# Performance work log

Measured on AMD Instinct MI355X. Metric: run time of the kernel, lower is better.

Reference implementation:

```python
import jax, jax.numpy as jnp
import numpy as np

DIM = 1024
RANK = 16


def setup_inputs() -> dict:
    key = jax.random.key(0)
    ks = jax.random.split(key, 9)
    s = 0.02
    return {
        "x": jax.random.normal(ks[0], (2, 4096, DIM), dtype=jnp.float32),
        "W_qkv": jax.random.normal(ks[1], (3 * DIM, DIM), dtype=jnp.float32) * s,
        "b_qkv": jax.random.normal(ks[2], (3 * DIM,), dtype=jnp.float32) * s,
        "A_q": jax.random.normal(ks[3], (RANK, DIM), dtype=jnp.float32) * s,
        "B_q": jax.random.normal(ks[4], (DIM, RANK), dtype=jnp.float32) * s,
        "A_k": jax.random.normal(ks[5], (RANK, DIM), dtype=jnp.float32) * s,
        "B_k": jax.random.normal(ks[6], (DIM, RANK), dtype=jnp.float32) * s,
        "A_v": jax.random.normal(ks[7], (RANK, DIM), dtype=jnp.float32) * s,
        "B_v": jax.random.normal(ks[8], (DIM, RANK), dtype=jnp.float32) * s,
        "alpha": jnp.float32(0.5),
    }


def reference(x, W_qkv, b_qkv, A_q, B_q, A_k, B_k, A_v, B_v, alpha):
    # base fused QKV projection: [B, S, 3*dim]
    qkv = jnp.einsum("bsd,od->bso", x, W_qkv) + b_qkv
    # low-rank adapters: x @ A.T @ B.T, rank=16
    lora_q = jnp.einsum("bsr,dr->bsd", jnp.einsum("bsd,rd->bsr", x, A_q), B_q)
    lora_k = jnp.einsum("bsr,dr->bsd", jnp.einsum("bsd,rd->bsr", x, A_k), B_k)
    lora_v = jnp.einsum("bsr,dr->bsd", jnp.einsum("bsd,rd->bsr", x, A_v), B_v)
    # scaled add into q/k/v slices (concat order matches torch slice layout)
    delta = jnp.concatenate([lora_q, lora_k, lora_v], axis=-1)
    return qkv + alpha * delta
```

## Files before the change

### kernel.cpp

```cpp
#include <hip/hip_runtime.h>
#include <stdint.h>

#define DIM    1024
#define RANK   16
#define M_TOT  8192
#define N_TOT  3072
#define K_TOT  1024

#define BM 256
#define BN 128
#define BK 64
#define NT (K_TOT / BK)

typedef __attribute__((ext_vector_type(8))) short  s8v;
typedef __attribute__((ext_vector_type(4))) float  f4v;

__device__ __forceinline__ unsigned short f2bf(float f) {
    union { float f; unsigned int u; } v; v.f = f;
    unsigned int u = v.u;
    u += 0x7FFFu + ((u >> 16) & 1u);
    return (unsigned short)(u >> 16);
}

__device__ __forceinline__ void gload_lds16(const unsigned short* g,
                                            unsigned short* l) {
    __builtin_amdgcn_global_load_lds(
        (const __attribute__((address_space(1))) void*)g,
        (__attribute__((address_space(3))) void*)l,
        16, 0, 0);
}

__global__ __launch_bounds__(256)
void prep(const float4* __restrict__ x, ushort4* __restrict__ xb,
          const float* __restrict__ W,
          const float* __restrict__ Aq, const float* __restrict__ Bq,
          const float* __restrict__ Ak, const float* __restrict__ Bk,
          const float* __restrict__ Av, const float* __restrict__ Bv,
          const float* __restrict__ alpha_p,
          unsigned short* __restrict__ Wb) {
    const int tid = threadIdx.x;
    if (blockIdx.x < 2048) {
        int i = blockIdx.x * 256 + tid;
        #pragma unroll
        for (int k = 0; k < 4; ++k) {
            float4 v = x[i];
            ushort4 o;
            o.x = f2bf(v.x); o.y = f2bf(v.y); o.z = f2bf(v.z); o.w = f2bf(v.w);
            xb[i] = o;
            i += 2048 * 256;
        }
    } else {
        const int bid2 = blockIdx.x - 2048;
        const int sel  = bid2 >> 6;
        const int rb   = bid2 & 63;
        const float* Am = (sel == 0) ? Aq : (sel == 1) ? Ak : Av;
        const float* Bm = (sel == 0) ? Bq : (sel == 1) ? Bk : Bv;

        __shared__ float sb[16][RANK];
        {
            const int row = rb * 16 + (tid >> 4);
            sb[tid >> 4][tid & 15] = alpha_p[0] * Bm[row * RANK + (tid & 15)];
        }
        __syncthreads();

        float4 a4[RANK];
        #pragma unroll
        for (int r = 0; r < RANK; ++r)
            a4[r] = ((const float4*)(Am + r * DIM))[tid];

        #pragma unroll
        for (int row = 0; row < 16; ++row) {
            const int o = sel * 1024 + rb * 16 + row;
            float4 w = ((const float4*)(W + (size_t)o * DIM))[tid];
            #pragma unroll
            for (int r = 0; r < RANK; ++r) {
                const float s = sb[row][r];
                w.x += s * a4[r].x; w.y += s * a4[r].y;
                w.z += s * a4[r].z; w.w += s * a4[r].w;
            }
            ushort4 ov;
            ov.x = f2bf(w.x); ov.y = f2bf(w.y); ov.z = f2bf(w.z); ov.w = f2bf(w.w);
            ((ushort4*)(Wb + (size_t)o * DIM))[tid] = ov;
        }
    }
}

__global__ __launch_bounds__(512, 2)
void gemm_bt(const unsigned short* __restrict__ Xb,
             const unsigned short* __restrict__ Wb,
             const float* __restrict__ bias,
             float* __restrict__ out) {
    __shared__ __align__(16) unsigned short As[2][BM * BK];
    __shared__ __align__(16) unsigned short Bs[2][BN * BK];

    const int tid  = threadIdx.x;
    const int wave = tid >> 6;
    const int lane = tid & 63;
    const int l15  = lane & 15;
    const int lq   = lane >> 4;
    const int wr   = wave >> 1;
    const int wc   = wave & 1;

    const int bid = blockIdx.x;
    const int xcd = bid & 7;
    const int s   = bid >> 3;
    const int bn  = s % 24;
    const int bm  = xcd * 4 + s / 24;

    const unsigned short* aptr[4];
    const unsigned short* bptr[2];
    int aoff[4], boff[2];
    #pragma unroll
    for (int u = 0; u < 4; ++u) {
        const int c   = wave * 4 + u;
        const int row = ((c >> 1) << 4) + l15;
        const int col = ((c & 1) << 5) + (lq << 3);
        aptr[u] = Xb + (size_t)(bm * BM + row) * K_TOT + col;
        aoff[u] = c * 512;
    }
    #pragma unroll
    for (int u = 0; u < 2; ++u) {
        const int c   = wave * 2 + u;
        const int row = ((c >> 1) << 4) + l15;
        const int col = ((c & 1) << 5) + (lq << 3);
        bptr[u] = Wb + (size_t)(bn * BN + row) * K_TOT + col;
        boff[u] = c * 512;
    }

    #pragma unroll
    for (int t = 0; t < 2; ++t) {
        #pragma unroll
        for (int u = 0; u < 4; ++u) gload_lds16(aptr[u] + t * BK, &As[t][aoff[u]]);
        #pragma unroll
        for (int u = 0; u < 2; ++u) gload_lds16(bptr[u] + t * BK, &Bs[t][boff[u]]);
    }

    f4v acc[4][4] = {};

    #define COMPUTE(curbuf)                                                      \
    {                                                                            \
        const s8v* Avp = (const s8v*)As[curbuf];                                 \
        const s8v* Bvp = (const s8v*)Bs[curbuf];                                 \
        _Pragma("unroll")                                                        \
        for (int t = 0; t < 2; ++t) {                                            \
            s8v af[4], bf[4];                                                    \
            _Pragma("unroll")                                                    \
            for (int i = 0; i < 4; ++i) {                                        \
                af[i] = Avp[((wr * 4 + i) * 2 + t) * 64 + lane];                 \
                bf[i] = Bvp[((wc * 4 + i) * 2 + t) * 64 + lane];                 \
            }                                                                    \
            _Pragma("unroll")                                                    \
            for (int i = 0; i < 4; ++i)                                          \
                _Pragma("unroll")                                                \
                for (int j = 0; j < 4; ++j)                                      \
                    acc[i][j] = __builtin_amdgcn_mfma_f32_16x16x32_bf16(         \
                        af[i], bf[j], acc[i][j], 0, 0, 0);                       \
        }                                                                        \
    }

    #pragma unroll 2
    for (int kt = 0; kt < NT - 2; ++kt) {
        const int cur = kt & 1;
        asm volatile("s_waitcnt vmcnt(6)" ::: "memory");
        __builtin_amdgcn_sched_barrier(0);
        __builtin_amdgcn_s_barrier();
        __builtin_amdgcn_sched_barrier(0);

        COMPUTE(cur);

        __builtin_amdgcn_sched_barrier(0);
        __builtin_amdgcn_s_barrier();
        __builtin_amdgcn_sched_barrier(0);

        #pragma unroll
        for (int u = 0; u < 4; ++u)
            gload_lds16(aptr[u] + (kt + 2) * BK, &As[cur][aoff[u]]);
        #pragma unroll
        for (int u = 0; u < 2; ++u)
            gload_lds16(bptr[u] + (kt + 2) * BK, &Bs[cur][boff[u]]);
    }

    asm volatile("s_waitcnt vmcnt(6)" ::: "memory");
    __builtin_amdgcn_sched_barrier(0);
    __builtin_amdgcn_s_barrier();
    __builtin_amdgcn_sched_barrier(0);
    COMPUTE(0);

    asm volatile("s_waitcnt vmcnt(0)" ::: "memory");
    __builtin_amdgcn_sched_barrier(0);
    __builtin_amdgcn_s_barrier();
    __builtin_amdgcn_sched_barrier(0);
    COMPUTE(1);
    #undef COMPUTE

    const int col_base = bn * BN + wc * 64;
    const int row_base = bm * BM + wr * 64 + lq * 4;
    #pragma unroll
    for (int j = 0; j < 4; ++j) {
        const int col = col_base + j * 16 + l15;
        const float bv = bias[col];
        #pragma unroll
        for (int i = 0; i < 4; ++i) {
            const int row = row_base + i * 16;
            #pragma unroll
            for (int r = 0; r < 4; ++r)
                out[(size_t)(row + r) * N_TOT + col] = acc[i][j][r] + bv;
        }
    }
}

extern "C" void kernel_launch(void* const* d_in, const int* in_sizes, int n_in,
                              void* d_out, int out_size, void* d_ws, size_t ws_size,
                              hipStream_t stream) {
    const float* x     = (const float*)d_in[0];
    const float* W     = (const float*)d_in[1];
    const float* b     = (const float*)d_in[2];
    const float* Aq    = (const float*)d_in[3];
    const float* Bq    = (const float*)d_in[4];
    const float* Ak    = (const float*)d_in[5];
    const float* Bk    = (const float*)d_in[6];
    const float* Av    = (const float*)d_in[7];
    const float* Bv    = (const float*)d_in[8];
    const float* alpha = (const float*)d_in[9];
    float* out = (float*)d_out;

    unsigned short* xb = (unsigned short*)d_ws;
    unsigned short* Wb = (unsigned short*)((char*)d_ws + (size_t)M_TOT * K_TOT * 2);

    prep<<<2048 + 192, 256, 0, stream>>>((const float4*)x, (ushort4*)xb,
                                         W, Aq, Bq, Ak, Bk, Av, Bv, alpha, Wb);

    gemm_bt<<<(M_TOT / BM) * (N_TOT / BN), 512, 0, stream>>>(xb, Wb, b, out);
}
```

Baseline: 254.0 us.

## Triple-buffer LDS and interleave async loads with MFMA sub-steps in GEMM

Switches the GEMM main loop from a double-buffered LDS ring to a three-stage ring, so the prefetch for tile q+2 can be issued while tile q is being consumed, with no barrier needed before overwriting. The global-to-LDS loads are split across the two K sub-steps and interleaved with the LDS fragment reads, and MFMA sections are wrapped in s_setprio for higher wave priority. This aims to hide memory latency and reduce barrier stalls. In exchange it raises LDS use to 144KB per block, which may limit occupancy to one block per CU, and the loop is no longer unrolled.

```diff
diff --git a/kernel.cpp b/kernel.cpp
--- a/kernel.cpp
+++ b/kernel.cpp
@@ -90,8 +90,8 @@
              const unsigned short* __restrict__ Wb,
              const float* __restrict__ bias,
              float* __restrict__ out) {
-    __shared__ __align__(16) unsigned short As[2][BM * BK];
-    __shared__ __align__(16) unsigned short Bs[2][BN * BK];
+    __shared__ __align__(16) unsigned short As[3][BM * BK];
+    __shared__ __align__(16) unsigned short Bs[3][BN * BK];
 
     const int tid  = threadIdx.x;
     const int wave = tid >> 6;
@@ -134,64 +134,86 @@
         #pragma unroll
         for (int u = 0; u < 2; ++u) gload_lds16(bptr[u] + t * BK, &Bs[t][boff[u]]);
     }
-
-    f4v acc[4][4] = {};
-
-    #define COMPUTE(curbuf)                                                      \
-    {                                                                            \
-        const s8v* Avp = (const s8v*)As[curbuf];                                 \
-        const s8v* Bvp = (const s8v*)Bs[curbuf];                                 \
-        _Pragma("unroll")                                                        \
-        for (int t = 0; t < 2; ++t) {                                            \
-            s8v af[4], bf[4];                                                    \
-            _Pragma("unroll")                                                    \
-            for (int i = 0; i < 4; ++i) {                                        \
-                af[i] = Avp[((wr * 4 + i) * 2 + t) * 64 + lane];                 \
-                bf[i] = Bvp[((wc * 4 + i) * 2 + t) * 64 + lane];                 \
-            }                                                                    \
-            _Pragma("unroll")                                                    \
-            for (int i = 0; i < 4; ++i)                                          \
-                _Pragma("unroll")                                                \
-                for (int j = 0; j < 4; ++j)                                      \
-                    acc[i][j] = __builtin_amdgcn_mfma_f32_16x16x32_bf16(         \
-                        af[i], bf[j], acc[i][j], 0, 0, 0);                       \
-        }                                                                        \
-    }
-
-    #pragma unroll 2
-    for (int kt = 0; kt < NT - 2; ++kt) {
-        const int cur = kt & 1;
-        asm volatile("s_waitcnt vmcnt(6)" ::: "memory");
-        __builtin_amdgcn_sched_barrier(0);
-        __builtin_amdgcn_s_barrier();
-        __builtin_amdgcn_sched_barrier(0);
-
-        COMPUTE(cur);
-
-        __builtin_amdgcn_sched_barrier(0);
-        __builtin_amdgcn_s_barrier();
-        __builtin_amdgcn_sched_barrier(0);
-
-        #pragma unroll
-        for (int u = 0; u < 4; ++u)
-            gload_lds16(aptr[u] + (kt + 2) * BK, &As[cur][aoff[u]]);
-        #pragma unroll
-        for (int u = 0; u < 2; ++u)
-            gload_lds16(bptr[u] + (kt + 2) * BK, &Bs[cur][boff[u]]);
-    }
-
     asm volatile("s_waitcnt vmcnt(6)" ::: "memory");
     __builtin_amdgcn_sched_barrier(0);
     __builtin_amdgcn_s_barrier();
     __builtin_amdgcn_sched_barrier(0);
-    COMPUTE(0);
-
-    asm volatile("s_waitcnt vmcnt(0)" ::: "memory");
-    __builtin_amdgcn_sched_barrier(0);
-    __builtin_amdgcn_s_barrier();
-    __builtin_amdgcn_sched_barrier(0);
-    COMPUTE(1);
-    #undef COMPUTE
+
+    f4v acc[4][4] = {};
+
+    #pragma unroll 1
+    for (int q = 0; q < NT; ++q) {
+        const int r    = q % 3;
+        const int r2   = (q + 2) % 3;
+        const int kg   = (q + 2) * BK;
+        const bool iss = (q + 2) < NT;
+        const s8v* Avp = (const s8v*)As[r];
+        const s8v* Bvp = (const s8v*)Bs[r];
+
+        {
+            s8v af[4], bf[4];
+            #pragma unroll
+            for (int i = 0; i < 4; ++i) {
+                af[i] = Avp[((wr * 4 + i) * 2 + 0) * 64 + lane];
+                bf[i] = Bvp[((wc * 4 + i) * 2 + 0) * 64 + lane];
+            }
+            if (iss) {
+                gload_lds16(aptr[0] + kg, &As[r2][aoff[0]]);
+                gload_lds16(aptr[1] + kg, &As[r2][aoff[1]]);
+                gload_lds16(bptr[0] + kg, &Bs[r2][boff[0]]);
+            }
+            __builtin_amdgcn_sched_barrier(0);
+            __builtin_amdgcn_s_barrier();
+            asm volatile("s_waitcnt lgkmcnt(0)" ::: "memory");
+            __builtin_amdgcn_sched_barrier(0);
+            __builtin_amdgcn_s_setprio(1);
+            #pragma unroll
+            for (int i = 0; i < 4; ++i)
+                #pragma unroll
+                for (int j = 0; j < 4; ++j)
+                    acc[i][j] = __builtin_amdgcn_mfma_f32_16x16x32_bf16(
+                        af[i], bf[j], acc[i][j], 0, 0, 0);
+            __builtin_amdgcn_s_setprio(0);
+            __builtin_amdgcn_sched_barrier(0);
+            __builtin_amdgcn_s_barrier();
+            __builtin_amdgcn_sched_barrier(0);
+        }
+
+        {
+            s8v af[4], bf[4];
+            #pragma unroll
+            for (int i = 0; i < 4; ++i) {
+                af[i] = Avp[((wr * 4 + i) * 2 + 1) * 64 + lane];
+                bf[i] = Bvp[((wc * 4 + i) * 2 + 1) * 64 + lane];
+            }
+            if (iss) {
+                gload_lds16(aptr[2] + kg, &As[r2][aoff[2]]);
+                gload_lds16(aptr[3] + kg, &As[r2][aoff[3]]);
+                gload_lds16(bptr[1] + kg, &Bs[r2][boff[1]]);
+            }
+            __builtin_amdgcn_sched_barrier(0);
+            __builtin_amdgcn_s_barrier();
+            asm volatile("s_waitcnt lgkmcnt(0)" ::: "memory");
+            __builtin_amdgcn_sched_barrier(0);
+            __builtin_amdgcn_s_setprio(1);
+            #pragma unroll
+            for (int i = 0; i < 4; ++i)
+                #pragma unroll
+                for (int j = 0; j < 4; ++j)
+                    acc[i][j] = __builtin_amdgcn_mfma_f32_16x16x32_bf16(
+                        af[i], bf[j], acc[i][j], 0, 0, 0);
+            __builtin_amdgcn_s_setprio(0);
+            __builtin_amdgcn_sched_barrier(0);
+            if (q < NT - 2) {
+                asm volatile("s_waitcnt vmcnt(6)" ::: "memory");
+            } else if (q == NT - 2) {
+                asm volatile("s_waitcnt vmcnt(0)" ::: "memory");
+            }
+            __builtin_amdgcn_sched_barrier(0);
+            __builtin_amdgcn_s_barrier();
+            __builtin_amdgcn_sched_barrier(0);
+        }
+    }
 
     const int col_base = bn * BN + wc * 64;
     const int row_base = bm * BM + wr * 64 + lq * 4;
```

New measurement: 233.4 us. 8.1% less time.

## Use 256x256 tiles with a 4-slot LDS ring and one barrier per step

Applied to the files above, without the earlier changes.

The GEMM tile grows from 256x128 to 256x256 and BK drops to 32. The two double buffers become one 4-slot LDS ring that keeps three stages of global-to-LDS loads in flight, with a single barrier per k-step. Waves are arranged 2x4, each computing a 128x64 sub-tile, and the MFMA bursts are raised with s_setprio. The aim is more reuse per LDS byte, fewer barriers and deeper latency hiding. The cost is 128KB of LDS, which allows only one block per CU, more accumulator registers per wave, and half as many blocks, which may hurt load balance across CUs.

```diff
diff --git a/kernel.cpp b/kernel.cpp
--- a/kernel.cpp
+++ b/kernel.cpp
@@ -8,9 +8,13 @@
 #define K_TOT  1024
 
 #define BM 256
-#define BN 128
-#define BK 64
+#define BN 256
+#define BK 32
 #define NT (K_TOT / BK)
+#define SLOT_H   16384
+#define SLOT_V   2048
+#define B_OFF_H  8192
+#define B_OFF_V  1024
 
 typedef __attribute__((ext_vector_type(8))) short  s8v;
 typedef __attribute__((ext_vector_type(4))) float  f4v;
@@ -90,117 +94,105 @@
              const unsigned short* __restrict__ Wb,
              const float* __restrict__ bias,
              float* __restrict__ out) {
-    __shared__ __align__(16) unsigned short As[2][BM * BK];
-    __shared__ __align__(16) unsigned short Bs[2][BN * BK];
+    __shared__ __align__(16) unsigned short S[4 * SLOT_H];
 
     const int tid  = threadIdx.x;
     const int wave = tid >> 6;
     const int lane = tid & 63;
     const int l15  = lane & 15;
     const int lq   = lane >> 4;
-    const int wr   = wave >> 1;
-    const int wc   = wave & 1;
+    const int wr   = wave >> 2;
+    const int wc   = wave & 3;
 
     const int bid = blockIdx.x;
     const int xcd = bid & 7;
     const int s   = bid >> 3;
-    const int bn  = s % 24;
-    const int bm  = xcd * 4 + s / 24;
-
-    const unsigned short* aptr[4];
+    const int bm  = xcd * 4 + s / 12;
+    const int bn  = s % 12;
+
+    const unsigned short* aptr[2];
     const unsigned short* bptr[2];
-    int aoff[4], boff[2];
-    #pragma unroll
-    for (int u = 0; u < 4; ++u) {
-        const int c   = wave * 4 + u;
-        const int row = ((c >> 1) << 4) + l15;
-        const int col = ((c & 1) << 5) + (lq << 3);
-        aptr[u] = Xb + (size_t)(bm * BM + row) * K_TOT + col;
-        aoff[u] = c * 512;
-    }
+    int aoff[2], boff[2];
     #pragma unroll
     for (int u = 0; u < 2; ++u) {
         const int c   = wave * 2 + u;
-        const int row = ((c >> 1) << 4) + l15;
-        const int col = ((c & 1) << 5) + (lq << 3);
+        const int row = c * 16 + l15;
+        const int col = lq << 3;
+        aptr[u] = Xb + (size_t)(bm * BM + row) * K_TOT + col;
         bptr[u] = Wb + (size_t)(bn * BN + row) * K_TOT + col;
-        boff[u] = c * 512;
-    }
-
-    #pragma unroll
-    for (int t = 0; t < 2; ++t) {
-        #pragma unroll
-        for (int u = 0; u < 4; ++u) gload_lds16(aptr[u] + t * BK, &As[t][aoff[u]]);
-        #pragma unroll
-        for (int u = 0; u < 2; ++u) gload_lds16(bptr[u] + t * BK, &Bs[t][boff[u]]);
-    }
-
-    f4v acc[4][4] = {};
-
-    #define COMPUTE(curbuf)                                                      \
-    {                                                                            \
-        const s8v* Avp = (const s8v*)As[curbuf];                                 \
-        const s8v* Bvp = (const s8v*)Bs[curbuf];                                 \
-        _Pragma("unroll")                                                        \
-        for (int t = 0; t < 2; ++t) {                                            \
-            s8v af[4], bf[4];                                                    \
-            _Pragma("unroll")                                                    \
-            for (int i = 0; i < 4; ++i) {                                        \
-                af[i] = Avp[((wr * 4 + i) * 2 + t) * 64 + lane];                 \
-                bf[i] = Bvp[((wc * 4 + i) * 2 + t) * 64 + lane];                 \
-            }                                                                    \
-            _Pragma("unroll")                                                    \
-            for (int i = 0; i < 4; ++i)                                          \
-                _Pragma("unroll")                                                \
-                for (int j = 0; j < 4; ++j)                                      \
-                    acc[i][j] = __builtin_amdgcn_mfma_f32_16x16x32_bf16(         \
-                        af[i], bf[j], acc[i][j], 0, 0, 0);                       \
-        }                                                                        \
-    }
-
-    #pragma unroll 2
-    for (int kt = 0; kt < NT - 2; ++kt) {
-        const int cur = kt & 1;
-        asm volatile("s_waitcnt vmcnt(6)" ::: "memory");
-        __builtin_amdgcn_sched_barrier(0);
-        __builtin_amdgcn_s_barrier();
-        __builtin_amdgcn_sched_barrier(0);
-
-        COMPUTE(cur);
-
-        __builtin_amdgcn_sched_barrier(0);
-        __builtin_amdgcn_s_barrier();
-        __builtin_amdgcn_sched_barrier(0);
-
-        #pragma unroll
-        for (int u = 0; u < 4; ++u)
-            gload_lds16(aptr[u] + (kt + 2) * BK, &As[cur][aoff[u]]);
-        #pragma unroll
-        for (int u = 0; u < 2; ++u)
-            gload_lds16(bptr[u] + (kt + 2) * BK, &Bs[cur][boff[u]]);
-    }
-
-    asm volatile("s_waitcnt vmcnt(6)" ::: "memory");
-    __builtin_amdgcn_sched_barrier(0);
-    __builtin_amdgcn_s_barrier();
-    __builtin_amdgcn_sched_barrier(0);
-    COMPUTE(0);
-
-    asm volatile("s_waitcnt vmcnt(0)" ::: "memory");
-    __builtin_amdgcn_sched_barrier(0);
-    __builtin_amdgcn_s_barrier();
-    __builtin_amdgcn_sched_barrier(0);
-    COMPUTE(1);
+        aoff[u] = c * 512;
+        boff[u] = B_OFF_H + c * 512;
+    }
+
+    #define STAGE(q)                                                         \
+    {                                                                        \
+        unsigned short* sl = &S[((q) & 3) * SLOT_H];                         \
+        const int kk = (q) * BK;                                             \
+        gload_lds16(aptr[0] + kk, sl + aoff[0]);                             \
+        gload_lds16(aptr[1] + kk, sl + aoff[1]);                             \
+        gload_lds16(bptr[0] + kk, sl + boff[0]);                             \
+        gload_lds16(bptr[1] + kk, sl + boff[1]);                             \
+    }
+
+    f4v acc[8][4] = {};
+
+    #define COMPUTE(q)                                                       \
+    {                                                                        \
+        const s8v* P = (const s8v*)S + ((q) & 3) * SLOT_V;                   \
+        s8v af[8], bf[4];                                                    \
+        _Pragma("unroll")                                                    \
+        for (int j = 0; j < 4; ++j)                                          \
+            bf[j] = P[B_OFF_V + (wc * 4 + j) * 64 + lane];                   \
+        _Pragma("unroll")                                                    \
+        for (int i = 0; i < 8; ++i)                                          \
+            af[i] = P[(wr * 8 + i) * 64 + lane];                             \
+        __builtin_amdgcn_s_setprio(1);                                       \
+        _Pragma("unroll")                                                    \
+        for (int i = 0; i < 8; ++i)                                          \
+            _Pragma("unroll")                                                \
+            for (int j = 0; j < 4; ++j)                                      \
+                acc[i][j] = __builtin_amdgcn_mfma_f32_16x16x32_bf16(         \
+                    af[i], bf[j], acc[i][j], 0, 0, 0);                       \
+        __builtin_amdgcn_s_setprio(0);                                       \
+    }
+
+    #define QSYNC(n)                                                         \
+    {                                                                        \
+        __builtin_amdgcn_sched_barrier(0);                                   \
+        asm volatile("s_waitcnt vmcnt(" #n ")" ::: "memory");                \
+        __builtin_amdgcn_s_barrier();                                        \
+        __builtin_amdgcn_sched_barrier(0);                                   \
+    }
+
+    STAGE(0); STAGE(1); STAGE(2);
+    QSYNC(8);
+
+    #pragma unroll 4
+    for (int q = 0; q < NT - 4; ++q) {
+        STAGE(q + 3);
+        COMPUTE(q);
+        QSYNC(8);
+    }
+    STAGE(NT - 1);
+    COMPUTE(NT - 4);
+    QSYNC(8);
+    COMPUTE(NT - 3);
+    QSYNC(4);
+    COMPUTE(NT - 2);
+    QSYNC(0);
+    COMPUTE(NT - 1);
+    #undef STAGE
     #undef COMPUTE
+    #undef QSYNC
 
     const int col_base = bn * BN + wc * 64;
-    const int row_base = bm * BM + wr * 64 + lq * 4;
+    const int row_base = bm * BM + wr * 128 + lq * 4;
     #pragma unroll
     for (int j = 0; j < 4; ++j) {
         const int col = col_base + j * 16 + l15;
         const float bv = bias[col];
         #pragma unroll
-        for (int i = 0; i < 4; ++i) {
+        for (int i = 0; i < 8; ++i) {
             const int row = row_base + i * 16;
             #pragma unroll
             for (int r = 0; r < 4; ++r)
```

Measured after the change: 225.8 us. -11.1%, faster.
